# Performance work log

Hardware: AMD Instinct MI355X
Metric: run time of the kernel (lower is better)

Reference implementation:

```python
import math
import jax, jax.numpy as jnp
from jax import lax
import numpy as np

WH, WW = 5, 9          # window_size
EH, EW = 3, 5          # expand_size = ((ws+1)//2)
NHEAD = 4
D = 512
PK, PS = 4, 4          # pool kernel / stride


def _valid_ind_rolled():
    m = np.ones((4, WH, WW), dtype=np.float32)
    m[0, :WH - EH, :WW - EW] = 0  # tl
    m[1, :WH - EH, EW:] = 0       # tr
    m[2, EH:, :WW - EW] = 0       # bl
    m[3, EH:, EW:] = 0            # br
    return np.nonzero(m.reshape(-1))[0]

VALID_IND = jnp.asarray(_valid_ind_rolled())  # (148,)


def _forward(x, masks, Wq, bq, Wk, bk, Wv, bv, Wp, bp, pool_w, pool_b):
    b, t, h, w, c = x.shape
    hd = c // NHEAD
    n_wh, n_ww = h // WH, w // WW
    n_win = n_wh * n_ww
    S = WH * WW  # tokens per window per frame (45)

    q = x @ Wq + bq
    k = x @ Wk + bk
    v = x @ Wv + bv

    def wp(a):  # window partition -> (b, n_win, nhead, t, S, hd)
        a = a.reshape(b, t, n_wh, WH, n_ww, WW, NHEAD, hd)
        a = a.transpose(0, 2, 4, 6, 1, 3, 5, 7)
        return a.reshape(b, n_win, NHEAD, t, S, hd)

    win_q, win_k, win_v = wp(q), wp(k), wp(v)

    # rolled (shifted) windows, gathered by the static valid-index buffer
    shifts = ((-EH, -EW), (-EH, EW), (EH, -EW), (EH, EW))
    roll_k = jnp.concatenate([wp(jnp.roll(k, s, axis=(2, 3))) for s in shifts], axis=4)[:, :, :, :, VALID_IND]
    roll_v = jnp.concatenate([wp(jnp.roll(v, s, axis=(2, 3))) for s in shifts], axis=4)[:, :, :, :, VALID_IND]

    # pooled global tokens via depthwise conv (kernel 4, stride 4)
    px = lax.conv_general_dilated(
        x.reshape(b * t, h, w, c), pool_w, (PS, PS), 'VALID',
        dimension_numbers=('NHWC', 'HWIO', 'NHWC'), feature_group_count=c) + pool_b
    ph, pw = px.shape[1], px.shape[2]
    P = ph * pw
    px = px.reshape(b, t, P, c)

    def pool_tok(a):  # (b,t,P,c) -> (b,1,nhead,t,P,hd)
        return a.reshape(b, t, P, NHEAD, hd).transpose(0, 3, 1, 2, 4)[:, None]

    pk = jnp.broadcast_to(pool_tok(px @ Wk + bk), (b, n_win, NHEAD, t, P, hd))
    pv = jnp.broadcast_to(pool_tok(px @ Wv + bv), (b, n_win, NHEAD, t, P, hd))

    win_k_full = jnp.concatenate([win_k, roll_k, pk], axis=4)  # (b,n_win,nh,t,K,hd)
    win_v_full = jnp.concatenate([win_v, roll_v, pv], axis=4)
    K = win_k_full.shape[4]

    # window-level mask: max-pool per window per frame, summed over frames, >0
    wmask = masks[..., 0].reshape(b, t, n_wh, WH, n_ww, WW).max(axis=(3, 5))
    wmask = wmask.reshape(b, t, n_win).sum(axis=1) > 0  # (b, n_win)

    scale = 1.0 / math.sqrt(hd)

    # dense spatiotemporal attention (used for masked windows)
    qd = win_q.reshape(b, n_win, NHEAD, t * S, hd)
    kd = win_k_full.reshape(b, n_win, NHEAD, t * K, hd)
    vd = win_v_full.reshape(b, n_win, NHEAD, t * K, hd)
    att_d = jax.nn.softmax(jnp.einsum('bnhqd,bnhkd->bnhqk', qd, kd) * scale, axis=-1)
    y_d = jnp.einsum('bnhqk,bnhkd->bnhqd', att_d, vd).reshape(b, n_win, NHEAD, t, S, hd)

    # per-frame local window attention (used for unmasked windows; keys = first S = window tokens)
    att_l = jax.nn.softmax(jnp.einsum('bnhtqd,bnhtkd->bnhtqk', win_q, win_k) * scale, axis=-1)
    y_l = jnp.einsum('bnhtqk,bnhtkd->bnhtqd', att_l, win_v)

    out = jnp.where(wmask[:, :, None, None, None, None], y_d, y_l)
    out = out.reshape(b, n_wh, n_ww, NHEAD, t, WH, WW, hd)
    out = out.transpose(0, 4, 1, 5, 2, 6, 3, 7).reshape(b, t, h, w, c)
    return out @ Wp + bp


def setup_inputs() -> dict:
    key = jax.random.key(0)
    ks = jax.random.split(key, 8)
    b, t, h, w = 1, 6, 40, 72
    x = jax.random.normal(ks[0], (b, t, h, w, D), dtype=jnp.float32)
    wm = (jax.random.uniform(ks[1], (b, t, h // WH, w // WW)) < 0.3).astype(jnp.float32)
    masks = jnp.repeat(jnp.repeat(wm, WH, axis=2), WW, axis=3)[..., None]
    s = 0.02

    def lin(kk):
        k1, k2 = jax.random.split(kk)
        return (jax.random.normal(k1, (D, D), jnp.float32) * s,
                jax.random.normal(k2, (D,), jnp.float32) * s)

    Wq, bq = lin(ks[2])
    Wk, bk = lin(ks[3])
    Wv, bv = lin(ks[4])
    Wp, bp = lin(ks[5])
    pool_w = jax.random.normal(ks[6], (PK, PK, 1, D), jnp.float32) * s
    pool_b = jax.random.normal(ks[7], (D,), jnp.float32) * s
    return {'x': x, 'masks': masks, 'Wq': Wq, 'bq': bq, 'Wk': Wk, 'bk': bk,
            'Wv': Wv, 'bv': bv, 'Wp': Wp, 'bp': bp, 'pool_w': pool_w, 'pool_b': pool_b}


def reference(x, masks, Wq, bq, Wk, bk, Wv, bv, Wp, bp, pool_w, pool_b):
    return _forward(x, masks, Wq, bq, Wk, bk, Wv, bv, Wp, bp, pool_w, pool_b)
```

## Files before the change

kernel.cpp:

```cpp
#include <hip/hip_runtime.h>

typedef unsigned short u16;
typedef unsigned int u32;
typedef __bf16 bf16x8 __attribute__((ext_vector_type(8)));
typedef float f32x4 __attribute__((ext_vector_type(4)));

#define TT 6
#define NTOK (6*40*72)
#define KTOT 373
#define NKEYS (TT*KTOT)
#define NCH2 35
#define SCALE 0.08838834764831845f
#define K_EXP2 0.12751743f

__device__ __forceinline__ float bf2f(u16 u){ u32 x = ((u32)u) << 16; return __builtin_bit_cast(float, x); }
__device__ __forceinline__ u16 f2bf(float f){ return __builtin_bit_cast(u16, (__bf16)f); }

__device__ __forceinline__ void gload16(const u16* g, u16* l){
  __builtin_amdgcn_global_load_lds(
      (const __attribute__((address_space(1))) void*)g,
      (__attribute__((address_space(3))) void*)l, 16, 0, 0);
}

__global__ __launch_bounds__(256) void convert_x(const float* __restrict__ src, u16* __restrict__ dst, int n4)
{
  int i = blockIdx.x * 256 + threadIdx.x;
  if (i >= n4) return;
  float4 v = *(const float4*)(src + (size_t)i * 4);
  u16 o[4] = {f2bf(v.x), f2bf(v.y), f2bf(v.z), f2bf(v.w)};
  *(uint2*)(dst + (size_t)i * 4) = *(const uint2*)o;
}

__global__ __launch_bounds__(256) void transpose_w(
    const float* __restrict__ w0, const float* __restrict__ w1,
    const float* __restrict__ w2, const float* __restrict__ w3, u16* __restrict__ out)
{
  __shared__ float tile[64][65];
  int m = blockIdx.z;
  const float* src = m == 0 ? w0 : (m == 1 ? w1 : (m == 2 ? w2 : w3));
  int kb = blockIdx.x * 64, nb = blockIdx.y * 64;
  int tid = threadIdx.x;
  int tx = tid & 63, ty = tid >> 6;
#pragma unroll
  for (int i = 0; i < 16; i++)
    tile[ty + 4*i][tx] = src[(size_t)(kb + ty + 4*i) * 512 + nb + tx];
  __syncthreads();
#pragma unroll
  for (int i = 0; i < 16; i++)
    out[m * 262144 + (size_t)(nb + ty + 4*i) * 512 + kb + tx] = f2bf(tile[tx][ty + 4*i]);
}

__global__ __launch_bounds__(256) void gemm_bias(
    const u16* __restrict__ A, const u16* __restrict__ wt,
    const float* __restrict__ b0, const float* __restrict__ b1, const float* __restrict__ b2,
    u16* __restrict__ c0, u16* __restrict__ c1, u16* __restrict__ c2, float* __restrict__ cf,
    int wo0, int wo1, int wo2, int M)
{
  __shared__ __align__(16) u16 sA[128*32];
  __shared__ __align__(16) u16 sB[128*32];
  int z = blockIdx.z;
  const u16* Bt = wt + (size_t)(z == 0 ? wo0 : (z == 1 ? wo1 : wo2)) * 262144;
  const float* bias = z == 0 ? b0 : (z == 1 ? b1 : b2);
  u16* Cout = z == 0 ? c0 : (z == 1 ? c1 : c2);
  int mbase = blockIdx.x * 128, nbase = blockIdx.y * 128;
  int tid = threadIdx.x, lane = tid & 63, wave = tid >> 6;
  int wm = (wave >> 1) * 64, wn = (wave & 1) * 64;
  int quad = lane >> 4, tr = lane & 15;
  int lrow = lane >> 2;
  int seg  = (lane & 3) ^ (lrow & 3);

  const u16* gA[2]; const u16* gB[2];
#pragma unroll
  for (int r = 0; r < 2; r++){
    gA[r] = A  + (size_t)(mbase + wave*32 + r*16 + lrow) * 512 + seg*8;
    gB[r] = Bt + (size_t)(nbase + wave*32 + r*16 + lrow) * 512 + seg*8;
  }
  u16* lA[2]; u16* lB[2];
#pragma unroll
  for (int r = 0; r < 2; r++){
    lA[r] = &sA[(wave*32 + r*16) * 32];
    lB[r] = &sB[(wave*32 + r*16) * 32];
  }

  f32x4 acc[4][4];
#pragma unroll
  for (int i = 0; i < 4; i++)
#pragma unroll
    for (int j = 0; j < 4; j++){ acc[i][j][0]=0.f; acc[i][j][1]=0.f; acc[i][j][2]=0.f; acc[i][j][3]=0.f; }

  int rcol = (quad ^ (tr & 3)) * 8;

  for (int k0 = 0; k0 < 512; k0 += 32){
    if (k0) __syncthreads();
#pragma unroll
    for (int r = 0; r < 2; r++){
      gload16(gA[r] + k0, lA[r]);
      gload16(gB[r] + k0, lB[r]);
    }
    __syncthreads();
    bf16x8 a[4], b[4];
#pragma unroll
    for (int i = 0; i < 4; i++) a[i] = *(const bf16x8*)(&sA[(wm + i*16 + tr)*32 + rcol]);
#pragma unroll
    for (int j = 0; j < 4; j++) b[j] = *(const bf16x8*)(&sB[(wn + j*16 + tr)*32 + rcol]);
#pragma unroll
    for (int i = 0; i < 4; i++)
#pragma unroll
      for (int j = 0; j < 4; j++)
        acc[i][j] = __builtin_amdgcn_mfma_f32_16x16x32_bf16(a[i], b[j], acc[i][j], 0, 0, 0);
  }

#pragma unroll
  for (int j = 0; j < 4; j++){
    int col = nbase + wn + j*16 + tr;
    float bv = bias[col];
#pragma unroll
    for (int i = 0; i < 4; i++)
#pragma unroll
      for (int r2 = 0; r2 < 4; r2++){
        int row = mbase + wm + i*16 + quad*4 + r2;
        if (row < M){
          float val = acc[i][j][r2] + bv;
          if (cf) cf[(size_t)row * 512 + col] = val;
          else    Cout[(size_t)row * 512 + col] = f2bf(val);
        }
      }
  }
}

__global__ __launch_bounds__(256) void pool_conv(
    const float* __restrict__ x, const float* __restrict__ pw,
    const float* __restrict__ pb, u16* __restrict__ px)
{
  int idx = blockIdx.x * 256 + threadIdx.x;
  int c = idx & 511, n = idx >> 9;
  int f = n / 180, rp = n % 180, ph = rp / 18, pwc = rp % 18;
  float acc = pb[c];
#pragma unroll
  for (int i = 0; i < 4; i++)
#pragma unroll
    for (int j = 0; j < 4; j++){
      int hh = ph*4 + i, ww = pwc*4 + j;
      acc += x[((size_t)((f*40 + hh)*72 + ww)) * 512 + c] * pw[(i*4 + j)*512 + c];
    }
  px[idx] = f2bf(acc);
}

__global__ void prep(const float* __restrict__ masks, int* __restrict__ wmask, int* __restrict__ vi)
{
  int tid = threadIdx.x;
  if (tid < 64) wmask[tid] = 0;
  __syncthreads();
  if (tid < 384){
    int f = tid / 64, win = tid & 63;
    int wi = win >> 3, wj = win & 7;
    int flag = 0;
    for (int p = 0; p < 45; p++){
      int hh = wi*5 + p/9, ww = wj*9 + p%9;
      if (masks[(f*40 + hh)*72 + ww] > 0.f) flag = 1;
    }
    if (flag) atomicOr(&wmask[win], 1);
  }
  if (tid == 448){
    int cnt = 0;
    for (int e = 0; e < 180; e++){
      int s = e / 45, pos = e % 45, pr = pos / 9, pc = pos % 9;
      bool inval = (s == 0 && pr < 2 && pc < 4) || (s == 1 && pr < 2 && pc >= 5) ||
                   (s == 2 && pr >= 3 && pc < 4) || (s == 3 && pr >= 3 && pc >= 5);
      if (!inval) vi[cnt++] = e;
    }
  }
}

__global__ __launch_bounds__(256) void build_idx(const int* __restrict__ vip, int* __restrict__ idxTab)
{
  int win = blockIdx.x, wi = win >> 3, wj = win & 7;
  for (int i = threadIdx.x; i < NKEYS; i += 256){
    int f = i / KTOT, slot = i - f * KTOT;
    int idx;
    if (slot < 45){
      int hh = wi*5 + slot/9, ww = wj*9 + slot%9;
      idx = ((f*40 + hh)*72 + ww) * 1024;
    } else if (slot < 193){
      int e = vip[slot - 45];
      int s2 = e / 45, pos = e - s2*45, pr = pos/9, pc = pos - pr*9;
      int hh = wi*5 + pr + ((s2 < 2) ? 3 : -3);
      int ww = wj*9 + pc + ((s2 & 1) ? -5 : 5);
      if (hh < 0) hh += 40; else if (hh >= 40) hh -= 40;
      if (ww < 0) ww += 72; else if (ww >= 72) ww -= 72;
      idx = ((f*40 + hh)*72 + ww) * 1024;
    } else {
      idx = ~((f*180 + (slot - 193)) * 1024);
    }
    idxTab[win * 2240 + i] = idx;
  }
}

__global__ __launch_bounds__(512) void attn_dense(
    const u16* __restrict__ qb, const u16* __restrict__ kb, const u16* __restrict__ vb,
    const u16* __restrict__ pkb, const u16* __restrict__ pvb,
    const int* __restrict__ wmaskp, const int* __restrict__ idxTab,
    u16* __restrict__ yb)
{
  __shared__ __align__(16) u16 sK[64][136];
  __shared__ __align__(16) u16 sVt[128][72];
  __shared__ __align__(16) u32 sPw[288][36];
  __shared__ int sIdx[2240];
  __shared__ float sDenX[32];

  int win = blockIdx.x, head = blockIdx.y;
  if (!wmaskp[win]) return;
  int wi = win >> 3, wj = win & 7;
  int tid = threadIdx.x, lane = tid & 63, wave = tid >> 6;
  int quad = lane >> 4, tr = lane & 15;

  if (tid < 32) sDenX[tid] = 0.f;
  {
    const int* g = idxTab + win * 2240;
    for (int i = tid; i < NKEYS; i += 512) sIdx[i] = g[i];
  }

  int mts[3] = {2*wave, 2*wave + 1, 16 + (wave >> 2)};
  bf16x8 qf[3][4];
#pragma unroll
  for (int im = 0; im < 3; im++){
    int row = mts[im]*16 + tr;
    int f = row / 48, r = row - f*48;
    bool vld = r < 45;
    int hh = wi*5 + r/9, ww = wj*9 + r%9;
    const u16* qp = qb + ((size_t)((f*40 + hh)*72 + ww))*512 + head*128;
#pragma unroll
    for (int kt = 0; kt < 4; kt++){
      uint4 v = make_uint4(0,0,0,0);
      if (vld) v = *(const uint4*)(qp + kt*32 + quad*8);
      qf[im][kt] = __builtin_bit_cast(bf16x8, v);
    }
  }

  f32x4 accv[2][8], accx[2];
#pragma unroll
  for (int m = 0; m < 2; m++)
#pragma unroll
    for (int nt = 0; nt < 8; nt++){ accv[m][nt][0]=0.f; accv[m][nt][1]=0.f; accv[m][nt][2]=0.f; accv[m][nt][3]=0.f; }
  accx[0][0]=0.f; accx[0][1]=0.f; accx[0][2]=0.f; accx[0][3]=0.f;
  accx[1][0]=0.f; accx[1][1]=0.f; accx[1][2]=0.f; accx[1][3]=0.f;
  float dacc[2] = {0.f, 0.f};
  float daccx = 0.f;

  __syncthreads();

  int upair = tid & 31, dgv = tid >> 5;
  const char* kb2  = (const char*)kb  + head*256 + (tid & 15)*16;
  const char* pkb2 = (const char*)pkb + head*256 + (tid & 15)*16;
  const char* vb2  = (const char*)vb  + head*256 + dgv*16;
  const char* pvb2 = (const char*)pvb + head*256 + dgv*16;

  uint4 pfk[2], pfv[2];
  auto pref = [&](int ch){
#pragma unroll
    for (int r = 0; r < 2; r++){ pfk[r] = make_uint4(0,0,0,0); pfv[r] = make_uint4(0,0,0,0); }
    if (ch < NCH2){
      int base = ch * 64;
#pragma unroll
      for (int r = 0; r < 2; r++){
        int jg = base + (tid >> 4) + 32*r;
        if (jg < NKEYS){
          int off = sIdx[jg];
          pfk[r] = *(const uint4*)(off >= 0 ? kb2 + off : pkb2 + ~off);
        }
      }
#pragma unroll
      for (int r = 0; r < 2; r++){
        int jg = base + 2*upair + r;
        if (jg < NKEYS){
          int off = sIdx[jg];
          pfv[r] = *(const uint4*)(off >= 0 ? vb2 + off : pvb2 + ~off);
        }
      }
    }
  };
  pref(0);

  for (int ch = 0; ch < NCH2; ch++){
    __syncthreads();
#pragma unroll
    for (int r = 0; r < 2; r++)
      *(uint4*)(&sK[(tid >> 4) + 32*r][(tid & 15)*8]) = pfk[r];
    {
      u32 va[4] = {pfv[0].x, pfv[0].y, pfv[0].z, pfv[0].w};
      u32 vbp[4] = {pfv[1].x, pfv[1].y, pfv[1].z, pfv[1].w};
#pragma unroll
      for (int jj = 0; jj < 8; jj++){
        u32 lo = (va[jj >> 1] >> (16*(jj & 1))) & 0xffffu;
        u32 hi = (vbp[jj >> 1] >> (16*(jj & 1))) & 0xffffu;
        ((u32*)&sVt[dgv*8 + jj][0])[upair] = lo | (hi << 16);
      }
    }
    __syncthreads();
    pref(ch + 1);

#pragma unroll
    for (int nt = 0; nt < 4; nt++){
      bf16x8 bk[4];
#pragma unroll
      for (int kt = 0; kt < 4; kt++) bk[kt] = *(const bf16x8*)(&sK[nt*16 + tr][kt*32 + quad*8]);
      int colb = ch*64 + nt*16 + quad*4;
#pragma unroll
      for (int m = 0; m < 2; m++){
        f32x4 s = {0.f, 0.f, 0.f, 0.f};
#pragma unroll
        for (int kt = 0; kt < 4; kt++) s = __builtin_amdgcn_mfma_f32_16x16x32_bf16(bk[kt], qf[m][kt], s, 0, 0, 0);
        float p[4];
#pragma unroll
        for (int r2 = 0; r2 < 4; r2++){
          p[r2] = (colb + r2 < NKEYS) ? __builtin_amdgcn_exp2f(s[r2] * K_EXP2) : 0.f;
          dacc[m] += p[r2];
        }
        uint2 w;
        w.x = (u32)f2bf(p[0]) | ((u32)f2bf(p[1]) << 16);
        w.y = (u32)f2bf(p[2]) | ((u32)f2bf(p[3]) << 16);
        *(uint2*)(&sPw[(2*wave + m)*16 + tr][nt*8 + quad*2]) = w;
      }
      if (nt == (wave & 3)){
        f32x4 s = {0.f, 0.f, 0.f, 0.f};
#pragma unroll
        for (int kt = 0; kt < 4; kt++) s = __builtin_amdgcn_mfma_f32_16x16x32_bf16(bk[kt], qf[2][kt], s, 0, 0, 0);
        float p[4];
#pragma unroll
        for (int r2 = 0; r2 < 4; r2++){
          p[r2] = (colb + r2 < NKEYS) ? __builtin_amdgcn_exp2f(s[r2] * K_EXP2) : 0.f;
          daccx += p[r2];
        }
        uint2 w;
        w.x = (u32)f2bf(p[0]) | ((u32)f2bf(p[1]) << 16);
        w.y = (u32)f2bf(p[2]) | ((u32)f2bf(p[3]) << 16);
        *(uint2*)(&sPw[(16 + (wave >> 2))*16 + tr][nt*8 + quad*2]) = w;
      }
    }
    __syncthreads();

#pragma unroll
    for (int kt2 = 0; kt2 < 2; kt2++){
      bf16x8 a0 = *(const bf16x8*)(&sPw[(2*wave)*16 + tr][kt2*16 + quad*4]);
      bf16x8 a1 = *(const bf16x8*)(&sPw[(2*wave + 1)*16 + tr][kt2*16 + quad*4]);
      bf16x8 ax = *(const bf16x8*)(&sPw[(16 + (wave >> 2))*16 + tr][kt2*16 + quad*4]);
#pragma unroll
      for (int nt = 0; nt < 8; nt++){
        bf16x8 bv = *(const bf16x8*)(&sVt[nt*16 + tr][kt2*32 + quad*8]);
        accv[0][nt] = __builtin_amdgcn_mfma_f32_16x16x32_bf16(a0, bv, accv[0][nt], 0, 0, 0);
        accv[1][nt] = __builtin_amdgcn_mfma_f32_16x16x32_bf16(a1, bv, accv[1][nt], 0, 0, 0);
      }
      int he0 = (wave & 3)*2;
      bf16x8 bx0 = *(const bf16x8*)(&sVt[he0*16 + tr][kt2*32 + quad*8]);
      bf16x8 bx1 = *(const bf16x8*)(&sVt[(he0+1)*16 + tr][kt2*32 + quad*8]);
      accx[0] = __builtin_amdgcn_mfma_f32_16x16x32_bf16(ax, bx0, accx[0], 0, 0, 0);
      accx[1] = __builtin_amdgcn_mfma_f32_16x16x32_bf16(ax, bx1, accx[1], 0, 0, 0);
    }
  }

  float dred[2];
#pragma unroll
  for (int m = 0; m < 2; m++){
    float d = dacc[m];
    d += __shfl_xor(d, 16, 64); d += __shfl_xor(d, 32, 64);
    dred[m] = d;
  }
  {
    float d = daccx;
    d += __shfl_xor(d, 16, 64); d += __shfl_xor(d, 32, 64);
    if (lane < 16) atomicAdd(&sDenX[(wave >> 2)*16 + lane], d);
  }
  __syncthreads();

#pragma unroll
  for (int m = 0; m < 2; m++){
#pragma unroll
    for (int r2 = 0; r2 < 4; r2++){
      float dinvv = 1.f / __shfl(dred[m], quad*4 + r2, 64);
      int row = (2*wave + m)*16 + quad*4 + r2;
      int f = row / 48, r = row - f*48;
      if (r < 45){
        int hh = wi*5 + r/9, ww = wj*9 + r%9;
        size_t base = ((size_t)((f*40 + hh)*72 + ww))*512 + head*128;
#pragma unroll
        for (int nt = 0; nt < 8; nt++)
          yb[base + nt*16 + tr] = f2bf(accv[m][nt][r2] * dinvv);
      }
    }
  }
  {
    int e = 16 + (wave >> 2), he0 = (wave & 3)*2;
#pragma unroll
    for (int r2 = 0; r2 < 4; r2++){
      int row = e*16 + quad*4 + r2;
      int f = row / 48, r = row - f*48;
      if (r < 45){
        float dinvv = 1.f / sDenX[(e - 16)*16 + quad*4 + r2];
        int hh = wi*5 + r/9, ww = wj*9 + r%9;
        size_t base = ((size_t)((f*40 + hh)*72 + ww))*512 + head*128;
        yb[base + he0*16 + tr]       = f2bf(accx[0][r2] * dinvv);
        yb[base + (he0 + 1)*16 + tr] = f2bf(accx[1][r2] * dinvv);
      }
    }
  }
}

__device__ __forceinline__ const u16* key_src_local(int slot, int qf, int wi, int wj, int head,
    const u16* __restrict__ tokbuf)
{
  int hh = wi*5 + slot/9, ww = wj*9 + slot%9;
  return tokbuf + ((size_t)((qf*40 + hh)*72 + ww)) * 512 + head * 128;
}

__global__ __launch_bounds__(256) void attn_local(
    const u16* __restrict__ qb, const u16* __restrict__ kb, const u16* __restrict__ vb,
    const int* __restrict__ wmaskp, u16* __restrict__ yb)
{
  __shared__ __align__(16) u16 sQ[48][136];
  __shared__ __align__(16) u16 sK[64][136];
  __shared__ __align__(16) u16 sVt[128][72];
  __shared__ __align__(16) u16 sP[48][72];
  __shared__ float sDen[48];

  int win = blockIdx.x, head = blockIdx.y, qf = blockIdx.z;
  if (wmaskp[win]) return;
  int wi = win >> 3, wj = win & 7;
  int tid = threadIdx.x, lane = tid & 63, wave = tid >> 6;
  int quad = lane >> 4, tr = lane & 15;

  if (tid < 48) sDen[tid] = 0.f;

#pragma unroll
  for (int r = 0; r < 3; r++){
    int u = tid + 256 * r;
    int row = u >> 4, dg = u & 15;
    uint4 val = make_uint4(0,0,0,0);
    if (row < 45){
      int hh = wi*5 + row/9, ww = wj*9 + row%9;
      val = *(const uint4*)(qb + ((size_t)((qf*40 + hh)*72 + ww)) * 512 + head*128 + dg*8);
    }
    *(uint4*)(&sQ[row][dg * 8]) = val;
  }

  const int nkeys = 45;
  f32x4 acc[3][2];
#pragma unroll
  for (int a = 0; a < 3; a++)
#pragma unroll
    for (int b = 0; b < 2; b++){ acc[a][b][0]=0.f; acc[a][b][1]=0.f; acc[a][b][2]=0.f; acc[a][b][3]=0.f; }

#pragma unroll
  for (int r = 0; r < 4; r++){
    int u = tid + 256 * r;
    int key = u >> 4, dg = u & 15;
    uint4 val = make_uint4(0,0,0,0);
    if (key < nkeys) val = *(const uint4*)(key_src_local(key, qf, wi, wj, head, kb) + dg * 8);
    *(uint4*)(&sK[key][dg * 8]) = val;
  }
#pragma unroll
  for (int r = 0; r < 4; r++){
    int u = tid + 256 * r;
    int key = u & 63, dg = u >> 6;
    uint4 val = make_uint4(0,0,0,0);
    if (key < nkeys) val = *(const uint4*)(key_src_local(key, qf, wi, wj, head, vb) + dg * 8);
    u32 vv[4] = {val.x, val.y, val.z, val.w};
#pragma unroll
    for (int q2 = 0; q2 < 4; q2++){
      sVt[dg*8 + q2*2][key]     = (u16)(vv[q2] & 0xffff);
      sVt[dg*8 + q2*2 + 1][key] = (u16)(vv[q2] >> 16);
    }
  }
  __syncthreads();

#pragma unroll
  for (int mt = 0; mt < 3; mt++){
    f32x4 sacc = {0.f, 0.f, 0.f, 0.f};
#pragma unroll
    for (int kt = 0; kt < 4; kt++){
      bf16x8 a = *(const bf16x8*)(&sQ[mt*16 + tr][kt*32 + quad*8]);
      bf16x8 b = *(const bf16x8*)(&sK[wave*16 + tr][kt*32 + quad*8]);
      sacc = __builtin_amdgcn_mfma_f32_16x16x32_bf16(a, b, sacc, 0, 0, 0);
    }
    int colg = wave * 16 + tr;
    float pr4[4];
#pragma unroll
    for (int r2 = 0; r2 < 4; r2++){
      float p = (colg < nkeys) ? __builtin_amdgcn_exp2f(sacc[r2] * K_EXP2) : 0.f;
      sP[mt*16 + quad*4 + r2][wave*16 + tr] = f2bf(p);
      pr4[r2] = p;
    }
#pragma unroll
    for (int r2 = 0; r2 < 4; r2++){
      float ps = pr4[r2];
      ps += __shfl_xor(ps, 1, 64);
      ps += __shfl_xor(ps, 2, 64);
      ps += __shfl_xor(ps, 4, 64);
      ps += __shfl_xor(ps, 8, 64);
      if (tr == 0) atomicAdd(&sDen[mt*16 + quad*4 + r2], ps);
    }
  }
  __syncthreads();

#pragma unroll
  for (int mt = 0; mt < 3; mt++)
#pragma unroll
    for (int nt = 0; nt < 2; nt++)
#pragma unroll
      for (int kt = 0; kt < 2; kt++){
        bf16x8 a = *(const bf16x8*)(&sP[mt*16 + tr][kt*32 + quad*8]);
        bf16x8 b = *(const bf16x8*)(&sVt[wave*32 + nt*16 + tr][kt*32 + quad*8]);
        acc[mt][nt] = __builtin_amdgcn_mfma_f32_16x16x32_bf16(a, b, acc[mt][nt], 0, 0, 0);
      }
  __syncthreads();

#pragma unroll
  for (int mt = 0; mt < 3; mt++)
#pragma unroll
    for (int r2 = 0; r2 < 4; r2++){
      int row = mt*16 + quad*4 + r2;
      if (row < 45){
        float dinv = 1.0f / sDen[row];
        int hh = wi*5 + row/9, ww = wj*9 + row%9;
        size_t base = ((size_t)((qf*40 + hh)*72 + ww)) * 512 + head * 128;
#pragma unroll
        for (int nt = 0; nt < 2; nt++){
          int col = wave*32 + nt*16 + tr;
          yb[base + col] = f2bf(acc[mt][nt][r2] * dinv);
        }
      }
    }
}

extern "C" void kernel_launch(void* const* d_in, const int* in_sizes, int n_in,
                              void* d_out, int out_size, void* d_ws, size_t ws_size,
                              hipStream_t stream)
{
  const float* x     = (const float*)d_in[0];
  const float* masks = (const float*)d_in[1];
  const float* Wq = (const float*)d_in[2];  const float* bq = (const float*)d_in[3];
  const float* Wk = (const float*)d_in[4];  const float* bk = (const float*)d_in[5];
  const float* Wv = (const float*)d_in[6];  const float* bv = (const float*)d_in[7];
  const float* Wp = (const float*)d_in[8];  const float* bp = (const float*)d_in[9];
  const float* pw = (const float*)d_in[10]; const float* pb = (const float*)d_in[11];
  float* out = (float*)d_out;

  char* ws = (char*)d_ws;
  size_t off = 0;
  auto alloc = [&](size_t bytes) -> char* {
    char* p = ws + off; off += (bytes + 255) & ~(size_t)255; return p;
  };
  u16* wt    = (u16*)alloc((size_t)4 * 512 * 512 * 2);
  u16* xbf   = (u16*)alloc((size_t)NTOK * 512 * 2);
  u16* qbuf  = (u16*)alloc((size_t)NTOK * 512 * 2);
  u16* kbuf  = (u16*)alloc((size_t)NTOK * 512 * 2);
  u16* vbuf  = (u16*)alloc((size_t)NTOK * 512 * 2);
  u16* pxbuf = (u16*)alloc((size_t)1080 * 512 * 2);
  u16* pkbuf = (u16*)alloc((size_t)1080 * 512 * 2);
  u16* pvbuf = (u16*)alloc((size_t)1080 * 512 * 2);
  u16* ybuf  = (u16*)alloc((size_t)NTOK * 512 * 2);
  int* wmaskb = (int*)alloc(64 * 4);
  int* vib    = (int*)alloc(148 * 4);
  int* idxTabb = (int*)alloc((size_t)64 * 2240 * 4);

  convert_x<<<dim3((NTOK*512/4 + 255)/256), 256, 0, stream>>>(x, xbf, NTOK*512/4);
  transpose_w<<<dim3(8, 8, 4), 256, 0, stream>>>(Wq, Wk, Wv, Wp, wt);
  gemm_bias<<<dim3(135, 4, 3), 256, 0, stream>>>(xbf, wt, bq, bk, bv, qbuf, kbuf, vbuf, nullptr, 0, 1, 2, NTOK);
  pool_conv<<<dim3(2160), 256, 0, stream>>>(x, pw, pb, pxbuf);
  gemm_bias<<<dim3(9, 4, 2), 256, 0, stream>>>(pxbuf, wt, bk, bv, bv, pkbuf, pvbuf, pvbuf, nullptr, 1, 2, 2, 1080);
  prep<<<dim3(1), 512, 0, stream>>>(masks, wmaskb, vib);
  build_idx<<<dim3(64), 256, 0, stream>>>(vib, idxTabb);
  attn_dense<<<dim3(64, 4), 512, 0, stream>>>(qbuf, kbuf, vbuf, pkbuf, pvbuf, wmaskb, idxTabb, ybuf);
  attn_local<<<dim3(64, 4, 6), 256, 0, stream>>>(qbuf, kbuf, vbuf, wmaskb, ybuf);
  gemm_bias<<<dim3(135, 4, 1), 256, 0, stream>>>(ybuf, wt, bp, bp, bp, nullptr, nullptr, nullptr, out, 3, 3, 3, NTOK);
}
```

Measured before the change: 386.1 us.

## Fuse Q/K/V projections into one GEMM sharing the A tile

Adds a gemm_qkv kernel in which each block loads one A (x) tile and computes all three Q, K, V outputs, keeping 3x4x4 MFMA accumulators per wave. This removes the triple re-read of x and cuts the grid from 1620 to 540 blocks. The cost is much higher register pressure (192 accumulator floats per lane) and fewer blocks, which could reduce occupancy and latency hiding on the 256-CU device.

```diff
diff --git a/kernel.cpp b/kernel.cpp
--- a/kernel.cpp
+++ b/kernel.cpp
@@ -48,6 +48,94 @@
 #pragma unroll
   for (int i = 0; i < 16; i++)
     out[m * 262144 + (size_t)(nb + ty + 4*i) * 512 + kb + tx] = f2bf(tile[tx][ty + 4*i]);
+}
+
+__global__ __launch_bounds__(256) void gemm_qkv(
+    const u16* __restrict__ A, const u16* __restrict__ wt,
+    const float* __restrict__ bq, const float* __restrict__ bk, const float* __restrict__ bv,
+    u16* __restrict__ cq, u16* __restrict__ ck, u16* __restrict__ cv, int M)
+{
+  __shared__ __align__(16) u16 sA[128*32];
+  __shared__ __align__(16) u16 sB[3][128*32];
+  int mbase = blockIdx.x * 128, nbase = blockIdx.y * 128;
+  int tid = threadIdx.x, lane = tid & 63, wave = tid >> 6;
+  int wm = (wave >> 1) * 64, wn = (wave & 1) * 64;
+  int quad = lane >> 4, tr = lane & 15;
+  int lrow = lane >> 2;
+  int seg  = (lane & 3) ^ (lrow & 3);
+
+  const u16* gA[2]; const u16* gB[3][2];
+#pragma unroll
+  for (int r = 0; r < 2; r++){
+    gA[r] = A + (size_t)(mbase + wave*32 + r*16 + lrow) * 512 + seg*8;
+#pragma unroll
+    for (int z = 0; z < 3; z++)
+      gB[z][r] = wt + (size_t)z * 262144 + (size_t)(nbase + wave*32 + r*16 + lrow) * 512 + seg*8;
+  }
+  u16* lA[2]; u16* lB[3][2];
+#pragma unroll
+  for (int r = 0; r < 2; r++){
+    lA[r] = &sA[(wave*32 + r*16) * 32];
+#pragma unroll
+    for (int z = 0; z < 3; z++)
+      lB[z][r] = &sB[z][(wave*32 + r*16) * 32];
+  }
+
+  f32x4 acc[3][4][4];
+#pragma unroll
+  for (int z = 0; z < 3; z++)
+#pragma unroll
+    for (int i = 0; i < 4; i++)
+#pragma unroll
+      for (int j = 0; j < 4; j++){ acc[z][i][j][0]=0.f; acc[z][i][j][1]=0.f; acc[z][i][j][2]=0.f; acc[z][i][j][3]=0.f; }
+
+  int rcol = (quad ^ (tr & 3)) * 8;
+
+  for (int k0 = 0; k0 < 512; k0 += 32){
+    if (k0) __syncthreads();
+#pragma unroll
+    for (int r = 0; r < 2; r++){
+      gload16(gA[r] + k0, lA[r]);
+#pragma unroll
+      for (int z = 0; z < 3; z++)
+        gload16(gB[z][r] + k0, lB[z][r]);
+    }
+    __syncthreads();
+    bf16x8 a[4];
+#pragma unroll
+    for (int i = 0; i < 4; i++) a[i] = *(const bf16x8*)(&sA[(wm + i*16 + tr)*32 + rcol]);
+#pragma unroll
+    for (int z = 0; z < 3; z++){
+      bf16x8 b[4];
+#pragma unroll
+      for (int j = 0; j < 4; j++) b[j] = *(const bf16x8*)(&sB[z][(wn + j*16 + tr)*32 + rcol]);
+#pragma unroll
+      for (int i = 0; i < 4; i++)
+#pragma unroll
+        for (int j = 0; j < 4; j++)
+          acc[z][i][j] = __builtin_amdgcn_mfma_f32_16x16x32_bf16(a[i], b[j], acc[z][i][j], 0, 0, 0);
+    }
+  }
+
+  const float* const biasp[3] = {bq, bk, bv};
+  u16* const outp[3] = {cq, ck, cv};
+#pragma unroll
+  for (int z = 0; z < 3; z++){
+    u16* Cout = outp[z];
+#pragma unroll
+    for (int j = 0; j < 4; j++){
+      int col = nbase + wn + j*16 + tr;
+      float bv2 = biasp[z][col];
+#pragma unroll
+      for (int i = 0; i < 4; i++)
+#pragma unroll
+        for (int r2 = 0; r2 < 4; r2++){
+          int row = mbase + wm + i*16 + quad*4 + r2;
+          if (row < M)
+            Cout[(size_t)row * 512 + col] = f2bf(acc[z][i][j][r2] + bv2);
+        }
+    }
+  }
 }
 
 __global__ __launch_bounds__(256) void gemm_bias(
@@ -564,7 +652,7 @@
 
   convert_x<<<dim3((NTOK*512/4 + 255)/256), 256, 0, stream>>>(x, xbf, NTOK*512/4);
   transpose_w<<<dim3(8, 8, 4), 256, 0, stream>>>(Wq, Wk, Wv, Wp, wt);
-  gemm_bias<<<dim3(135, 4, 3), 256, 0, stream>>>(xbf, wt, bq, bk, bv, qbuf, kbuf, vbuf, nullptr, 0, 1, 2, NTOK);
+  gemm_qkv<<<dim3(135, 4), 256, 0, stream>>>(xbf, wt, bq, bk, bv, qbuf, kbuf, vbuf, NTOK);
   pool_conv<<<dim3(2160), 256, 0, stream>>>(x, pw, pb, pxbuf);
   gemm_bias<<<dim3(9, 4, 2), 256, 0, stream>>>(pxbuf, wt, bk, bv, bv, pkbuf, pvbuf, pvbuf, nullptr, 1, 2, 2, 1080);
   prep<<<dim3(1), 512, 0, stream>>>(masks, wmaskb, vib);
```

After: 430.9 us. 1.12x slower.
